# Optimization experiments

Measured on AMD Instinct MI355X. Metric: run time of the kernel, lower is better.

Reference implementation:

```python
import jax, jax.numpy as jnp
import numpy as np

EPS = 1e-6
ROPE_THETA = 10000.0


def rmsnorm(x, w):
    return x * jax.lax.rsqrt(jnp.mean(x * x, axis=-1, keepdims=True) + EPS) * w


def rope(q, k, seq_len, head_dim):
    # rotate-half RoPE. q,k: [b, h, s, d]
    half = head_dim // 2
    inv_freq = 1.0 / (ROPE_THETA ** (jnp.arange(0, half, dtype=jnp.float32) / half))
    t = jnp.arange(seq_len, dtype=jnp.float32)
    freqs = jnp.outer(t, inv_freq)                      # [s, d/2]
    cos = jnp.concatenate([jnp.cos(freqs)] * 2, axis=-1)  # [s, d]
    sin = jnp.concatenate([jnp.sin(freqs)] * 2, axis=-1)

    def rot(x):
        x1, x2 = x[..., :half], x[..., half:]
        return jnp.concatenate([-x2, x1], axis=-1)

    return q * cos + rot(q) * sin, k * cos + rot(k) * sin


def setup_inputs() -> dict:
    key = jax.random.key(0)
    ks = jax.random.split(key, 8)
    B, S, D, E, F = 4, 2048, 1024, 8, 4096
    sd = 0.02
    return {
        "x": jax.random.normal(ks[0], (B, S, D), dtype=jnp.float32),
        "mapped_tokens": jax.random.randint(ks[1], (B, S), 0, E, dtype=jnp.int32),
        "rms1_w": jnp.ones((D,), dtype=jnp.float32),
        "wqkv": jax.random.normal(ks[2], (D, 3 * D), dtype=jnp.float32) * sd,
        "wo": jax.random.normal(ks[3], (D, D), dtype=jnp.float32) * sd,
        "rms2_w": jnp.ones((D,), dtype=jnp.float32),
        "w1": jax.random.normal(ks[4], (E, D, F), dtype=jnp.float32) * sd,
        "w2": jax.random.normal(ks[5], (E, F, D), dtype=jnp.float32) * sd,
    }


def attention(x, wqkv, wo, num_heads=16):
    B, S, D = x.shape
    hd = D // num_heads
    qkv = x @ wqkv                                       # [b, s, 3D]
    q, k, v = jnp.split(qkv, 3, axis=-1)
    def heads(t):
        return t.reshape(B, S, num_heads, hd).transpose(0, 2, 1, 3)  # [b,h,s,d]
    q, k, v = heads(q), heads(k), heads(v)
    q, k = rope(q, k, S, hd)
    scores = jnp.einsum("bhqd,bhkd->bhqk", q, k) / jnp.sqrt(jnp.float32(hd))
    causal = jnp.tril(jnp.ones((S, S), dtype=bool))
    scores = jnp.where(causal, scores, jnp.finfo(scores.dtype).min)
    attn = jax.nn.softmax(scores, axis=-1)
    out = jnp.einsum("bhqk,bhkd->bhqd", attn, v)
    out = out.transpose(0, 2, 1, 3).reshape(B, S, D)
    return out @ wo


def moe_hash_ffn(x, mapped_tokens, w1, w2):
    # hash-routed MoE: each token goes to exactly one expert given by mapped_tokens
    B, S, D = x.shape
    E = w1.shape[0]
    xf = x.reshape(B * S, D)
    mt = mapped_tokens.reshape(B * S)
    out = jnp.zeros_like(xf)
    for e in range(E):  # small fixed expert count
        y = jax.nn.gelu(xf @ w1[e]) @ w2[e]
        out = out + jnp.where((mt == e)[:, None], y, 0.0)
    return out.reshape(B, S, D)


def reference(x, mapped_tokens, rms1_w, wqkv, wo, rms2_w, w1, w2):
    h = x + attention(rmsnorm(x, rms1_w), wqkv, wo)
    out = h + moe_hash_ffn(rmsnorm(h, rms2_w), mapped_tokens, w1, w2)
    return out
```

## Files before the change

### kernel.cpp

```cpp
#include <hip/hip_runtime.h>
#include <hip/hip_bf16.h>
#include <stdint.h>

typedef __hip_bfloat16 bf16;
typedef __attribute__((ext_vector_type(8))) short bf16x8;
typedef __attribute__((ext_vector_type(4))) float f32x4;
typedef __attribute__((ext_vector_type(16))) float f32x16;
typedef unsigned int u32;

static constexpr int Bsz = 4, S = 2048, D = 1024, E = 8, F = 4096, NH = 16, HD = 64;
static constexpr int TOK = Bsz * S;
static constexpr int SLOTS = TOK + E * 256;

#define DEV __device__ __forceinline__

DEV void async16(const bf16* g, bf16* l) {
  __builtin_amdgcn_global_load_lds((const __attribute__((address_space(1))) u32*)g,
                                   (__attribute__((address_space(3))) u32*)l, 16, 0, 0);
}

DEV u32 lds_off(const bf16* p) {
  return (u32)(uintptr_t)(__attribute__((address_space(3))) bf16*)p;
}

DEV bf16x8 dsr128(u32 addr) {
  bf16x8 d;
  asm volatile("ds_read_b128 %0, %1" : "=v"(d) : "v"(addr));
  return d;
}

DEV float gelu_fast(float x) {
  const float z = 0.7978845608028654f * (x + 0.044715f * x * x * x);
  return x / (1.f + __expf(-2.f * z));
}


__global__ void cvt_transpose(const float* __restrict__ in, bf16* __restrict__ out, int R, int C) {
  __shared__ float t[64][65];
  const size_t zoff = (size_t)blockIdx.z * R * C;
  const int c0 = blockIdx.x * 64, r0 = blockIdx.y * 64;
  const int tid = threadIdx.x;
  const int lrow = tid >> 4, lcol = (tid & 15) * 4;
#pragma unroll
  for (int p = 0; p < 4; ++p) {
    const int r = lrow + p * 16;
    const float4 v = *(const float4*)(in + zoff + (size_t)(r0 + r) * C + c0 + lcol);
    t[r][lcol] = v.x; t[r][lcol + 1] = v.y; t[r][lcol + 2] = v.z; t[r][lcol + 3] = v.w;
  }
  __syncthreads();
  const int ow = tid >> 3, je = (tid & 7) * 8;
#pragma unroll
  for (int p = 0; p < 2; ++p) {
    const int oc = ow + p * 32;
    union { bf16x8 v; bf16 b[8]; } o8;
#pragma unroll
    for (int j = 0; j < 8; ++j) o8.b[j] = __float2bfloat16(t[je + j][oc]);
    *(bf16x8*)(out + zoff + (size_t)(c0 + oc) * R + r0 + je) = o8.v;
  }
}

__global__ void rope_tables(float* __restrict__ cosT, float* __restrict__ sinT) {
  const int s = blockIdx.x * 2 + (threadIdx.x >> 5);
  const int i = threadIdx.x & 31;
  const float inv_freq = powf(10000.f, -(float)i / 32.f);
  const float ang = (float)s * inv_freq;
  cosT[s * 32 + i] = cosf(ang);
  sinT[s * 32 + i] = sinf(ang);
}

__global__ void rmsnorm_k(const float* __restrict__ x, const float* __restrict__ w, bf16* __restrict__ out) {
  const size_t row = blockIdx.x;
  const int tid = threadIdx.x;
  const float4 v = *(const float4*)(x + row * D + tid * 4);
  float ss = v.x * v.x + v.y * v.y + v.z * v.z + v.w * v.w;
#pragma unroll
  for (int off = 1; off < 64; off <<= 1) ss += __shfl_xor(ss, off);
  __shared__ float red[4];
  if ((tid & 63) == 0) red[tid >> 6] = ss;
  __syncthreads();
  const float inv = rsqrtf((red[0] + red[1] + red[2] + red[3]) * (1.f / D) + 1e-6f);
  const float4 wv = *(const float4*)(w + tid * 4);
  union { ushort4 u; bf16 b[4]; } o;
  o.b[0] = __float2bfloat16(v.x * inv * wv.x);
  o.b[1] = __float2bfloat16(v.y * inv * wv.y);
  o.b[2] = __float2bfloat16(v.z * inv * wv.z);
  o.b[3] = __float2bfloat16(v.w * inv * wv.w);
  *(ushort4*)((unsigned short*)out + row * D + tid * 4) = o.u;
}

__global__ void route_init(int* counts, int* cursors, int* perm) {
  const int i = blockIdx.x * 256 + threadIdx.x;
  if (i < E) { counts[i] = 0; cursors[i] = 0; }
  if (i < SLOTS) perm[i] = -1;
}
__global__ void route_count(const int* __restrict__ mt, int* counts) {
  const int i = blockIdx.x * 256 + threadIdx.x;
  if (i < TOK) atomicAdd(&counts[mt[i]], 1);
}
__global__ void route_offsets(const int* __restrict__ counts, int* aoff) {
  if (threadIdx.x == 0) {
    int off = 0; aoff[0] = 0;
    for (int e = 0; e < E; ++e) { off += (counts[e] + 255) & ~255; aoff[e + 1] = off; }
  }
}
__global__ void route_scatter(const int* __restrict__ mt, const int* __restrict__ aoff,
                              int* cursors, int* perm) {
  const int i = blockIdx.x * 256 + threadIdx.x;
  if (i < TOK) { const int e = mt[i]; perm[aoff[e] + atomicAdd(&cursors[e], 1)] = i; }
}

__global__ __launch_bounds__(512) void qkv8p(
    const bf16* __restrict__ A, const bf16* __restrict__ Bt,
    const float* __restrict__ c_t, const float* __restrict__ s_t,
    bf16* __restrict__ o_q, bf16* __restrict__ o_k, bf16* __restrict__ o_v) {
  constexpr int K = 1024, NT = K / 64;
  __shared__ __align__(16) bf16 LA[2][256 * 64];
  __shared__ __align__(16) bf16 LB[2][256 * 64];
  const int tid = threadIdx.x;
  const int lane = tid & 63, wv = tid >> 6;
  const int wm = wv >> 2, wn = wv & 3;
  const int rl = lane & 15, kg = lane >> 4;
  const int gx = gridDim.x;
  const int nwg = gx * gridDim.y;
  int bid = blockIdx.y * gx + blockIdx.x;
  bid = (bid & 7) * (nwg >> 3) + (bid >> 3);
  const int nbase = (bid % gx) * 256, mbase = (bid / gx) * 256;
  f32x4 acc[8][4] = {};
  const int srow = tid >> 3;
  const int sc = (tid & 7) ^ ((srow >> 1) & 7);
  const bf16* Ag = A + (size_t)(mbase + srow) * K + sc * 8;
  const bf16* Bg = Bt + (size_t)(nbase + srow) * K + sc * 8;

  auto stage = [&](int t, int h) {
    const int buf = t & 1;
    const int mat = h >> 1, rh = h & 1;
    const bf16* src = (mat ? Bg : Ag) + (size_t)(rh * 128) * K + t * 64;
    bf16* dst = (mat ? &LB[buf][0] : &LA[buf][0]) + rh * 128 * 64 + tid * 8;
    async16(src, dst);
    async16(src + (size_t)64 * K, dst + 64 * 64);
  };

  bf16x8 bfr[4];
  auto phaseC = [&](int t, int ks, int mih, bool loadB) {
    const int buf = t & 1;
    const u32 ab = lds_off(&LA[buf][0]);
    const u32 bb = lds_off(&LB[buf][0]);
    bf16x8 af[4];
#pragma unroll
    for (int mi = 0; mi < 4; ++mi) {
      const int row = wm * 128 + mih * 64 + mi * 16 + rl;
      const u32 ph = (u32)((ks * 4 + kg) ^ ((row >> 1) & 7));
      af[mi] = dsr128(ab + (u32)row * 128 + ph * 16);
    }
    if (loadB) {
#pragma unroll
      for (int ni = 0; ni < 4; ++ni) {
        const int row = wn * 64 + ni * 16 + rl;
        const u32 ph = (u32)((ks * 4 + kg) ^ ((row >> 1) & 7));
        bfr[ni] = dsr128(bb + (u32)row * 128 + ph * 16);
      }
    }
    asm volatile("s_waitcnt lgkmcnt(0)" ::: "memory");
    __builtin_amdgcn_sched_barrier(0);
    __builtin_amdgcn_s_setprio(1);
#pragma unroll
    for (int mi = 0; mi < 4; ++mi)
#pragma unroll
      for (int ni = 0; ni < 4; ++ni)
        acc[mih * 4 + mi][ni] =
            __builtin_amdgcn_mfma_f32_16x16x32_bf16(af[mi], bfr[ni], acc[mih * 4 + mi][ni], 0, 0, 0);
    __builtin_amdgcn_s_setprio(0);
  };

  stage(0, 0); stage(0, 1); stage(0, 2); stage(0, 3);
  for (int t = 0; t < NT; ++t) {
    const bool more = (t + 1 < NT);
#pragma unroll
    for (int p = 0; p < 4; ++p) {
      if (p == 0) {
        if (more) {
          stage(t + 1, 0);
          asm volatile("s_waitcnt vmcnt(2)" ::: "memory");
        } else {
          asm volatile("s_waitcnt vmcnt(0)" ::: "memory");
        }
        __builtin_amdgcn_s_barrier();
        __builtin_amdgcn_sched_barrier(0);
      } else if (more) {
        stage(t + 1, p);
      }
      phaseC(t, p >> 1, p & 1, (p & 1) == 0);
      __builtin_amdgcn_s_barrier();
      __builtin_amdgcn_sched_barrier(0);
    }
  }

  const int colbase = nbase + wn * 64;
  const int part = colbase >> 10;
  const int head = (colbase & 1023) >> 6;
#pragma unroll
  for (int ai = 0; ai < 8; ++ai) {
    const int rowoff = (ai >> 2) * 64 + (ai & 3) * 16;
#pragma unroll
    for (int r = 0; r < 4; ++r) {
      const int grow = mbase + wm * 128 + rowoff + kg * 4 + r;
      const int bb = grow >> 11, sp = grow & (S - 1);
      if (part == 2) {
#pragma unroll
        for (int ni = 0; ni < 4; ++ni) {
          const int d = ni * 16 + rl;
          o_v[((size_t)(bb * NH + head) * HD + d) * S + sp] = __float2bfloat16(acc[ai][ni][r]);
        }
      } else {
        bf16* dst = (part == 0) ? o_q : o_k;
        const size_t base = ((size_t)(bb * NH + head) * S + sp) * HD;
#pragma unroll
        for (int np = 0; np < 2; ++np) {
          const int i = np * 16 + rl;
          const float c = c_t[sp * 32 + i];
          const float sn = s_t[sp * 32 + i];
          const float lo = acc[ai][np][r];
          const float hi = acc[ai][np + 2][r];
          dst[base + i] = __float2bfloat16(lo * c - hi * sn);
          dst[base + i + 32] = __float2bfloat16(hi * c + lo * sn);
        }
      }
    }
  }
}

template <int EPI, int K>
__global__ __launch_bounds__(512) void ffn4p(
    const bf16* __restrict__ A, const bf16* __restrict__ Bt,
    const int* __restrict__ aoff, long long estride,
    bf16* __restrict__ o_act,
    const int* __restrict__ perm, const float* __restrict__ hres,
    float* __restrict__ o_out) {
  constexpr int NT = K / 64;
  __shared__ __align__(16) bf16 LA[2][256 * 64];
  __shared__ __align__(16) bf16 LB[2][256 * 64];
  const int tid = threadIdx.x;
  const int lane = tid & 63, wv = tid >> 6;
  const int wm = wv >> 2, wn = wv & 3;
  const int rl = lane & 15, kg = lane >> 4;
  const int gx = gridDim.x;
  const int nwg = gx * gridDim.y;
  int bid = blockIdx.y * gx + blockIdx.x;
  bid = (bid & 7) * (nwg >> 3) + (bid >> 3);
  const int nbase = (bid % gx) * 256, mbase = (bid / gx) * 256;
  if (mbase >= aoff[E]) return;
  int e = 0;
#pragma unroll
  for (int t = 0; t < E - 1; ++t) e += (mbase >= aoff[t + 1]) ? 1 : 0;
  const bf16* Btp = Bt + (size_t)e * estride;

  f32x4 acc[8][4] = {};
  const int srow = tid >> 3;
  const int sc = (tid & 7) ^ ((srow >> 1) & 7);
  const bf16* Agr[4];
#pragma unroll
  for (int c = 0; c < 4; ++c) {
    int slot = mbase + c * 64 + srow;
    if constexpr (EPI == 2) { const int pt = perm[slot]; slot = (pt < 0) ? 0 : pt; }
    Agr[c] = A + (size_t)slot * K + sc * 8;
  }
  const bf16* Bg = Btp + (size_t)(nbase + srow) * K + sc * 8;

  auto stage = [&](int t, int h) {
    const int buf = t & 1;
    const int mat = h >> 1, rh = h & 1;
    bf16* dst = (mat ? &LB[buf][0] : &LA[buf][0]) + rh * 128 * 64 + tid * 8;
    if (mat == 0) {
      async16(Agr[rh * 2] + t * 64, dst);
      async16(Agr[rh * 2 + 1] + t * 64, dst + 64 * 64);
    } else {
      const bf16* src = Bg + (size_t)(rh * 128) * K + t * 64;
      async16(src, dst);
      async16(src + (size_t)64 * K, dst + 64 * 64);
    }
  };

  bf16x8 bfr[4];
  auto phaseC = [&](int t, int ks, int mih, bool loadB) {
    const int buf = t & 1;
    const u32 ab = lds_off(&LA[buf][0]);
    const u32 bb = lds_off(&LB[buf][0]);
    bf16x8 af[4];
#pragma unroll
    for (int mi = 0; mi < 4; ++mi) {
      const int row = wm * 128 + mih * 64 + mi * 16 + rl;
      const u32 ph = (u32)((ks * 4 + kg) ^ ((row >> 1) & 7));
      af[mi] = dsr128(ab + (u32)row * 128 + ph * 16);
    }
    if (loadB) {
#pragma unroll
      for (int ni = 0; ni < 4; ++ni) {
        const int row = wn * 64 + ni * 16 + rl;
        const u32 ph = (u32)((ks * 4 + kg) ^ ((row >> 1) & 7));
        bfr[ni] = dsr128(bb + (u32)row * 128 + ph * 16);
      }
    }
    asm volatile("s_waitcnt lgkmcnt(0)" ::: "memory");
    __builtin_amdgcn_sched_barrier(0);
    __builtin_amdgcn_s_setprio(1);
#pragma unroll
    for (int mi = 0; mi < 4; ++mi)
#pragma unroll
      for (int ni = 0; ni < 4; ++ni)
        acc[mih * 4 + mi][ni] =
            __builtin_amdgcn_mfma_f32_16x16x32_bf16(af[mi], bfr[ni], acc[mih * 4 + mi][ni], 0, 0, 0);
    __builtin_amdgcn_s_setprio(0);
  };

  stage(0, 0); stage(0, 1); stage(0, 2); stage(0, 3);
  for (int t = 0; t < NT; ++t) {
    const bool more = (t + 1 < NT);
#pragma unroll
    for (int p = 0; p < 4; ++p) {
      if (p == 0) {
        if (more) {
          stage(t + 1, 0);
          asm volatile("s_waitcnt vmcnt(2)" ::: "memory");
        } else {
          asm volatile("s_waitcnt vmcnt(0)" ::: "memory");
        }
        __builtin_amdgcn_s_barrier();
        __builtin_amdgcn_sched_barrier(0);
      } else if (more) {
        stage(t + 1, p);
      }
      phaseC(t, p >> 1, p & 1, (p & 1) == 0);
      __builtin_amdgcn_s_barrier();
      __builtin_amdgcn_sched_barrier(0);
    }
  }

#pragma unroll
  for (int ai = 0; ai < 8; ++ai) {
    const int rowoff = (ai >> 2) * 64 + (ai & 3) * 16;
#pragma unroll
    for (int r = 0; r < 4; ++r) {
      const int grow = mbase + wm * 128 + rowoff + kg * 4 + r;
#pragma unroll
      for (int ni = 0; ni < 4; ++ni) {
        const int gcol = nbase + wn * 64 + ni * 16 + rl;
        const float vv = acc[ai][ni][r];
        if constexpr (EPI == 2) {
          o_act[(size_t)grow * 4096 + gcol] = __float2bfloat16(gelu_fast(vv));
        } else {
          const int tk = perm[grow];
          if (tk >= 0) {
            const size_t ix = (size_t)tk * 1024 + gcol;
            o_out[ix] = hres[ix] + vv;
          }
        }
      }
    }
  }
}

template <int EPI, int BM>
__global__ __launch_bounds__(2 * BM) void gemm_bt(
    const bf16* __restrict__ A, const bf16* __restrict__ Bt, int M, int N, int K,
    const int* __restrict__ aoff, long long estride,
    const float* __restrict__ xres, float* __restrict__ o_h,
    bf16* __restrict__ o_act,
    const int* __restrict__ perm, const float* __restrict__ hres, float* __restrict__ o_out) {
  constexpr int WN = BM / 64;
  constexpr int MR = BM / 2;
  constexpr int M_FR = MR / 16;
  __shared__ __align__(16) bf16 As[2][BM * 32];
  __shared__ __align__(16) bf16 Bs[2][BM * 32];
  const int tid = threadIdx.x;
  const int lane = tid & 63, wv = tid >> 6;
  const int wm = wv / WN, wn = wv % WN;
  const int rl = lane & 15, kg = lane >> 4;
  const int gx = gridDim.x;
  const int nwg = gx * gridDim.y;
  int bid = blockIdx.y * gx + blockIdx.x;
  bid = (bid & 7) * (nwg >> 3) + (bid >> 3);
  const int nbase = (bid % gx) * BM, mbase = (bid / gx) * BM;
  const bf16* Btp = Bt;
  if constexpr (EPI >= 2) {
    int e = 0;
#pragma unroll
    for (int t = 0; t < E - 1; ++t) e += (mbase >= aoff[t + 1]) ? 1 : 0;
    Btp = Bt + (size_t)e * estride;
  }
  f32x4 acc[M_FR][4] = {};
  const int srow = tid >> 2;
  const int sc = (tid & 3) ^ ((srow >> 1) & 3);
  const bf16* Agp[2];
#pragma unroll
  for (int c = 0; c < 2; ++c) {
    int rowslot = mbase + c * MR + srow;
    if constexpr (EPI == 2) {
      const int t = perm[rowslot];
      rowslot = (t < 0) ? 0 : t;
    }
    Agp[c] = A + (size_t)rowslot * K + sc * 8;
  }
  const bf16* Bg = Btp + (size_t)(nbase + srow) * K + sc * 8;

  auto stage = [&](int bi, int ko) {
#pragma unroll
    for (int c = 0; c < 2; ++c) {
      async16(Agp[c] + ko, &As[bi][c * MR * 32 + wv * 512]);
      async16(Bg + (size_t)(c * MR) * K + ko, &Bs[bi][c * MR * 32 + wv * 512]);
    }
  };
  auto compute = [&](int bi) {
    bf16x8 af[M_FR], bfr[4];
#pragma unroll
    for (int mi = 0; mi < M_FR; ++mi) {
      const int row = wm * MR + mi * 16 + rl;
      af[mi] = *(const bf16x8*)&As[bi][row * 32 + ((kg ^ ((row >> 1) & 3))) * 8];
    }
#pragma unroll
    for (int ni = 0; ni < 4; ++ni) {
      const int row = wn * 64 + ni * 16 + rl;
      bfr[ni] = *(const bf16x8*)&Bs[bi][row * 32 + ((kg ^ ((row >> 1) & 3))) * 8];
    }
#pragma unroll
    for (int mi = 0; mi < M_FR; ++mi)
#pragma unroll
      for (int ni = 0; ni < 4; ++ni)
        acc[mi][ni] = __builtin_amdgcn_mfma_f32_16x16x32_bf16(af[mi], bfr[ni], acc[mi][ni], 0, 0, 0);
  };

  const int nk = K >> 5;
  stage(0, 0);
  __syncthreads();
  for (int kb = 0; kb < nk; ++kb) {
    if (kb + 1 < nk) stage((kb + 1) & 1, (kb + 1) * 32);
    compute(kb & 1);
    __syncthreads();
  }

#pragma unroll
  for (int mi = 0; mi < M_FR; ++mi) {
#pragma unroll
    for (int ni = 0; ni < 4; ++ni) {
#pragma unroll
      for (int r = 0; r < 4; ++r) {
        const int grow = mbase + wm * MR + mi * 16 + kg * 4 + r;
        const int gcol = nbase + wn * 64 + ni * 16 + rl;
        const float vv = acc[mi][ni][r];
        if constexpr (EPI == 1) {
          const size_t ix = (size_t)grow * 1024 + gcol;
          o_h[ix] = xres[ix] + vv;
        } else if constexpr (EPI == 2) {
          o_act[(size_t)grow * 4096 + gcol] = __float2bfloat16(gelu_fast(vv));
        } else {
          const int t = perm[grow];
          if (t >= 0) {
            const size_t ix = (size_t)t * 1024 + gcol;
            o_out[ix] = hres[ix] + vv;
          }
        }
      }
    }
  }
}

__global__ __launch_bounds__(128, 4) void attn_kernel(const bf16* __restrict__ Qb,
                                                      const bf16* __restrict__ Kb,
                                                      const bf16* __restrict__ Vt,
                                                      bf16* __restrict__ AO) {
  const int bh = blockIdx.x;
  const int w = threadIdx.x >> 6, lane = threadIdx.x & 63;
  const int q = lane & 31, hi = lane >> 5;
  const bf16* Qp = Qb + (size_t)bh * S * HD;
  const bf16* Kp = Kb + (size_t)bh * S * HD;
  const bf16* Vp = Vt + (size_t)bh * S * HD;
  const int b = bh >> 4, h = bh & 15;
  __shared__ __align__(16) bf16 Pl[2][4][32][16];
  const int qt = (S / 32 - 1) - (blockIdx.y * 2 + w);
  const int qrow0 = qt * 32;
  const float SC = 0.125f * 1.4426950408889634f;
  bf16x8 qf[4];
#pragma unroll
  for (int t = 0; t < 4; ++t)
    qf[t] = *(const bf16x8*)(Qp + (size_t)(qrow0 + q) * HD + t * 16 + hi * 8);
  f32x16 oa0 = {}, oa1 = {};
  float m = -INFINITY, l = 0.f;
  const int nt = (qt + 2) >> 1;
  for (int kt = 0; kt < nt; ++kt) {
    const int kvb = kt * 64;
    f32x16 sa0 = {}, sa1 = {};
#pragma unroll
    for (int t = 0; t < 4; ++t) {
      const bf16x8 kf0 = *(const bf16x8*)(Kp + (size_t)(kvb + q) * HD + t * 16 + hi * 8);
      sa0 = __builtin_amdgcn_mfma_f32_32x32x16_bf16(kf0, qf[t], sa0, 0, 0, 0);
    }
#pragma unroll
    for (int t = 0; t < 4; ++t) {
      const bf16x8 kf1 = *(const bf16x8*)(Kp + (size_t)(kvb + 32 + q) * HD + t * 16 + hi * 8);
      sa1 = __builtin_amdgcn_mfma_f32_32x32x16_bf16(kf1, qf[t], sa1, 0, 0, 0);
    }
#pragma unroll
    for (int r = 0; r < 16; ++r) {
      const int kloc = (r & 3) + 8 * (r >> 2) + 4 * hi;
      sa0[r] = (kvb + kloc > qrow0 + q) ? -3.0e38f : sa0[r] * SC;
      sa1[r] = (kvb + 32 + kloc > qrow0 + q) ? -3.0e38f : sa1[r] * SC;
    }
    float vm;
    {
      float a0 = fmaxf(fmaxf(sa0[0], sa0[1]), fmaxf(sa0[2], sa0[3]));
      float a1 = fmaxf(fmaxf(sa0[4], sa0[5]), fmaxf(sa0[6], sa0[7]));
      float a2 = fmaxf(fmaxf(sa0[8], sa0[9]), fmaxf(sa0[10], sa0[11]));
      float a3 = fmaxf(fmaxf(sa0[12], sa0[13]), fmaxf(sa0[14], sa0[15]));
      float b0 = fmaxf(fmaxf(sa1[0], sa1[1]), fmaxf(sa1[2], sa1[3]));
      float b1 = fmaxf(fmaxf(sa1[4], sa1[5]), fmaxf(sa1[6], sa1[7]));
      float b2 = fmaxf(fmaxf(sa1[8], sa1[9]), fmaxf(sa1[10], sa1[11]));
      float b3 = fmaxf(fmaxf(sa1[12], sa1[13]), fmaxf(sa1[14], sa1[15]));
      vm = fmaxf(fmaxf(fmaxf(a0, a1), fmaxf(a2, a3)), fmaxf(fmaxf(b0, b1), fmaxf(b2, b3)));
    }
    vm = fmaxf(vm, __shfl_xor(vm, 32));
    const bool grow = __any(vm > m);
    const float mn = grow ? fmaxf(m, vm) : m;
#pragma unroll
    for (int r = 0; r < 16; ++r) {
      sa0[r] = exp2f(sa0[r] - mn);
      sa1[r] = exp2f(sa1[r] - mn);
    }
    float ps;
    {
      float a0 = (sa0[0] + sa0[1]) + (sa0[2] + sa0[3]);
      float a1 = (sa0[4] + sa0[5]) + (sa0[6] + sa0[7]);
      float a2 = (sa0[8] + sa0[9]) + (sa0[10] + sa0[11]);
      float a3 = (sa0[12] + sa0[13]) + (sa0[14] + sa0[15]);
      float b0 = (sa1[0] + sa1[1]) + (sa1[2] + sa1[3]);
      float b1 = (sa1[4] + sa1[5]) + (sa1[6] + sa1[7]);
      float b2 = (sa1[8] + sa1[9]) + (sa1[10] + sa1[11]);
      float b3 = (sa1[12] + sa1[13]) + (sa1[14] + sa1[15]);
      ps = ((a0 + a1) + (a2 + a3)) + ((b0 + b1) + (b2 + b3));
    }
    ps += __shfl_xor(ps, 32);
    if (grow) {
      const float scs = exp2f(m - mn);
      l = l * scs + ps;
      m = mn;
#pragma unroll
      for (int r = 0; r < 16; ++r) { oa0[r] *= scs; oa1[r] *= scs; }
    } else {
      l += ps;
    }
#pragma unroll
    for (int g = 0; g < 8; ++g) {
      union { ushort4 u4; bf16 bb[4]; } pk;
#pragma unroll
      for (int j = 0; j < 4; ++j) {
        const int r = 4 * (g & 3) + j;
        pk.bb[j] = __float2bfloat16((g < 4) ? sa0[r] : sa1[r]);
      }
      *(ushort4*)&Pl[w][g >> 1][q][8 * (g & 1) + 4 * hi] = pk.u4;
    }
#pragma unroll
    for (int s2i = 0; s2i < 4; ++s2i) {
      const bf16x8 pf = *(const bf16x8*)&Pl[w][s2i][q][8 * hi];
      const bf16x8 vf0 = *(const bf16x8*)(Vp + (size_t)q * S + kvb + 16 * s2i + 8 * hi);
      const bf16x8 vf1 = *(const bf16x8*)(Vp + (size_t)(32 + q) * S + kvb + 16 * s2i + 8 * hi);
      oa0 = __builtin_amdgcn_mfma_f32_32x32x16_bf16(vf0, pf, oa0, 0, 0, 0);
      oa1 = __builtin_amdgcn_mfma_f32_32x32x16_bf16(vf1, pf, oa1, 0, 0, 0);
    }
  }
  const float invl = 1.f / l;
#pragma unroll
  for (int n = 0; n < 2; ++n) {
#pragma unroll
    for (int g = 0; g < 4; ++g) {
      union { ushort4 u4; bf16 bb[4]; } o4;
#pragma unroll
      for (int mi = 0; mi < 4; ++mi) {
        const float val = (n ? oa1[4 * g + mi] : oa0[4 * g + mi]) * invl;
        o4.bb[mi] = __float2bfloat16(val);
      }
      const int d = n * 32 + 8 * g + 4 * hi;
      *(ushort4*)&AO[((size_t)(b * S + qrow0 + q)) * D + h * HD + d] = o4.u4;
    }
  }
}

extern "C" void kernel_launch(void* const* d_in, const int* in_sizes, int n_in,
                              void* d_out, int out_size, void* d_ws, size_t ws_size,
                              hipStream_t stream) {
  const float* x = (const float*)d_in[0];
  const int* mt = (const int*)d_in[1];
  const float* rms1 = (const float*)d_in[2];
  const float* wqkv = (const float*)d_in[3];
  const float* wo = (const float*)d_in[4];
  const float* rms2 = (const float*)d_in[5];
  const float* w1 = (const float*)d_in[6];
  const float* w2 = (const float*)d_in[7];
  float* out = (float*)d_out;
  (void)in_sizes; (void)n_in; (void)out_size; (void)ws_size;

  char* ws = (char*)d_ws;
  size_t off = 0;
  auto alloc = [&](size_t b) { void* p = ws + off; off = (off + b + 255) & ~(size_t)255; return p; };
  bf16* wqkvT = (bf16*)alloc((size_t)3072 * 1024 * 2);
  bf16* woT   = (bf16*)alloc((size_t)1024 * 1024 * 2);
  bf16* w1T   = (bf16*)alloc((size_t)E * F * D * 2);
  bf16* w2T   = (bf16*)alloc((size_t)E * D * F * 2);
  float* cosT = (float*)alloc((size_t)S * 32 * 4);
  float* sinT = (float*)alloc((size_t)S * 32 * 4);
  float* hbuf = (float*)alloc((size_t)TOK * D * 4);
  bf16* xn2   = (bf16*)alloc((size_t)TOK * D * 2);
  int* counts  = (int*)alloc(E * 4);
  int* cursors = (int*)alloc(E * 4);
  int* aoff    = (int*)alloc((E + 1) * 4);
  int* perm    = (int*)alloc(SLOTS * 4);
  char* R = (char*)alloc((size_t)5 * TOK * D * 2);
  bf16* xn = (bf16*)R;
  bf16* qb = (bf16*)(R + (size_t)1 * TOK * D * 2);
  bf16* kb = (bf16*)(R + (size_t)2 * TOK * D * 2);
  bf16* vb = (bf16*)(R + (size_t)3 * TOK * D * 2);
  bf16* ao = (bf16*)(R + (size_t)4 * TOK * D * 2);
  bf16* act = (bf16*)R;

  cvt_transpose<<<dim3(3072 / 64, 1024 / 64, 1), 256, 0, stream>>>(wqkv, wqkvT, 1024, 3072);
  cvt_transpose<<<dim3(1024 / 64, 1024 / 64, 1), 256, 0, stream>>>(wo, woT, 1024, 1024);
  cvt_transpose<<<dim3(4096 / 64, 1024 / 64, E), 256, 0, stream>>>(w1, w1T, 1024, 4096);
  cvt_transpose<<<dim3(1024 / 64, 4096 / 64, E), 256, 0, stream>>>(w2, w2T, 4096, 1024);
  rope_tables<<<dim3(S / 2), 64, 0, stream>>>(cosT, sinT);
  route_init<<<dim3((SLOTS + 255) / 256), 256, 0, stream>>>(counts, cursors, perm);
  route_count<<<dim3(TOK / 256), 256, 0, stream>>>(mt, counts);
  route_offsets<<<dim3(1), 64, 0, stream>>>(counts, aoff);
  route_scatter<<<dim3(TOK / 256), 256, 0, stream>>>(mt, aoff, cursors, perm);
  rmsnorm_k<<<dim3(TOK), 256, 0, stream>>>(x, rms1, xn);
  qkv8p<<<dim3(3072 / 256, TOK / 256), 512, 0, stream>>>(
      xn, wqkvT, cosT, sinT, qb, kb, vb);
  attn_kernel<<<dim3(64, S / 64), 128, 0, stream>>>(qb, kb, vb, ao);
  gemm_bt<1, 128><<<dim3(1024 / 128, TOK / 128), 256, 0, stream>>>(
      ao, woT, TOK, 1024, 1024, nullptr, 0, x, hbuf, nullptr, nullptr, nullptr, nullptr);
  rmsnorm_k<<<dim3(TOK), 256, 0, stream>>>(hbuf, rms2, xn2);
  ffn4p<2, 1024><<<dim3(4096 / 256, SLOTS / 256), 512, 0, stream>>>(
      xn2, w1T, aoff, (long long)F * D, act, perm, nullptr, nullptr);
  ffn4p<3, 4096><<<dim3(1024 / 256, SLOTS / 256), 512, 0, stream>>>(
      act, w2T, aoff, (long long)D * F, nullptr, perm, hbuf, out);
}
```

Baseline: 708.4 us.

## Split-K FFN down-proj with atomics, reorder GEMM stage pipeline, fold softmax scale into Q

The FFN2 GEMM is split along K into four z-slices. Their partial results are accumulated with float atomicAdd into an output that the Wo GEMM epilogue pre-initialises with the residual, which raises block-level parallelism for the K=4096 GEMM. The qkv and FFN GEMM main loops are restructured to load B first and hold two B fragment register sets, with adjusted vmcnt waits. The attention softmax scale is folded into the Q epilogue, and causal masking is skipped for fully unmasked KV tiles. The atomics add contention and make the summation order nondeterministic.

```diff
diff --git a/kernel.cpp b/kernel.cpp
--- a/kernel.cpp
+++ b/kernel.cpp
@@ -133,15 +133,21 @@
 
   auto stage = [&](int t, int h) {
     const int buf = t & 1;
-    const int mat = h >> 1, rh = h & 1;
-    const bf16* src = (mat ? Bg : Ag) + (size_t)(rh * 128) * K + t * 64;
-    bf16* dst = (mat ? &LB[buf][0] : &LA[buf][0]) + rh * 128 * 64 + tid * 8;
-    async16(src, dst);
-    async16(src + (size_t)64 * K, dst + 64 * 64);
+    if (h < 2) {
+      const bf16* src = Bg + (size_t)(h * 128) * K + t * 64;
+      bf16* dst = &LB[buf][0] + h * 128 * 64 + tid * 8;
+      async16(src, dst);
+      async16(src + (size_t)64 * K, dst + 64 * 64);
+    } else {
+      const int rh = h - 2;
+      const bf16* src = Ag + (size_t)(rh * 64) * K + t * 64;
+      bf16* dst = &LA[buf][0] + rh * 64 * 64 + tid * 8;
+      async16(src, dst);
+      async16(src + (size_t)128 * K, dst + 128 * 64);
+    }
   };
 
-  bf16x8 bfr[4];
-  auto phaseC = [&](int t, int ks, int mih, bool loadB) {
+  auto phaseC = [&](int t, int ks, int mih, bf16x8 (&bfr)[4], bool loadB) {
     const int buf = t & 1;
     const u32 ab = lds_off(&LA[buf][0]);
     const u32 bb = lds_off(&LB[buf][0]);
@@ -172,32 +178,44 @@
     __builtin_amdgcn_s_setprio(0);
   };
 
+  bf16x8 bfr0[4], bfr1[4];
   stage(0, 0); stage(0, 1); stage(0, 2); stage(0, 3);
   for (int t = 0; t < NT; ++t) {
     const bool more = (t + 1 < NT);
-#pragma unroll
-    for (int p = 0; p < 4; ++p) {
-      if (p == 0) {
-        if (more) {
-          stage(t + 1, 0);
-          asm volatile("s_waitcnt vmcnt(2)" ::: "memory");
-        } else {
-          asm volatile("s_waitcnt vmcnt(0)" ::: "memory");
-        }
-        __builtin_amdgcn_s_barrier();
-        __builtin_amdgcn_sched_barrier(0);
-      } else if (more) {
-        stage(t + 1, p);
-      }
-      phaseC(t, p >> 1, p & 1, (p & 1) == 0);
-      __builtin_amdgcn_s_barrier();
-      __builtin_amdgcn_sched_barrier(0);
-    }
+    if (more) {
+      stage(t + 1, 0);
+      asm volatile("s_waitcnt vmcnt(4)" ::: "memory");
+    } else {
+      asm volatile("s_waitcnt vmcnt(2)" ::: "memory");
+    }
+    __builtin_amdgcn_s_barrier();
+    __builtin_amdgcn_sched_barrier(0);
+    phaseC(t, 0, 0, bfr0, true);
+    __builtin_amdgcn_s_barrier();
+    __builtin_amdgcn_sched_barrier(0);
+    if (more) stage(t + 1, 1);
+    phaseC(t, 1, 0, bfr1, true);
+    if (more) {
+      asm volatile("s_waitcnt vmcnt(4)" ::: "memory");
+    } else {
+      asm volatile("s_waitcnt vmcnt(0)" ::: "memory");
+    }
+    __builtin_amdgcn_s_barrier();
+    __builtin_amdgcn_sched_barrier(0);
+    if (more) stage(t + 1, 2);
+    phaseC(t, 0, 1, bfr0, false);
+    __builtin_amdgcn_s_barrier();
+    __builtin_amdgcn_sched_barrier(0);
+    if (more) stage(t + 1, 3);
+    phaseC(t, 1, 1, bfr1, false);
+    __builtin_amdgcn_s_barrier();
+    __builtin_amdgcn_sched_barrier(0);
   }
 
   const int colbase = nbase + wn * 64;
   const int part = colbase >> 10;
   const int head = (colbase & 1023) >> 6;
+  const float qs = (part == 0) ? 0.18033688011112042f : 1.f;
 #pragma unroll
   for (int ai = 0; ai < 8; ++ai) {
     const int rowoff = (ai >> 2) * 64 + (ai & 3) * 16;
@@ -221,8 +239,8 @@
           const float sn = s_t[sp * 32 + i];
           const float lo = acc[ai][np][r];
           const float hi = acc[ai][np + 2][r];
-          dst[base + i] = __float2bfloat16(lo * c - hi * sn);
-          dst[base + i + 32] = __float2bfloat16(hi * c + lo * sn);
+          dst[base + i] = __float2bfloat16((lo * c - hi * sn) * qs);
+          dst[base + i + 32] = __float2bfloat16((hi * c + lo * sn) * qs);
         }
       }
     }
@@ -231,11 +249,10 @@
 
 template <int EPI, int K>
 __global__ __launch_bounds__(512) void ffn4p(
-    const bf16* __restrict__ A, const bf16* __restrict__ Bt,
+    const bf16* __restrict__ A, const bf16* __restrict__ Bt, int lda,
     const int* __restrict__ aoff, long long estride,
     bf16* __restrict__ o_act,
-    const int* __restrict__ perm, const float* __restrict__ hres,
-    float* __restrict__ o_out) {
+    const int* __restrict__ perm, float* __restrict__ o_out) {
   constexpr int NT = K / 64;
   __shared__ __align__(16) bf16 LA[2][256 * 64];
   __shared__ __align__(16) bf16 LB[2][256 * 64];
@@ -249,6 +266,7 @@
   bid = (bid & 7) * (nwg >> 3) + (bid >> 3);
   const int nbase = (bid % gx) * 256, mbase = (bid / gx) * 256;
   if (mbase >= aoff[E]) return;
+  const size_t koff = (size_t)blockIdx.z * K;
   int e = 0;
 #pragma unroll
   for (int t = 0; t < E - 1; ++t) e += (mbase >= aoff[t + 1]) ? 1 : 0;
@@ -262,26 +280,26 @@
   for (int c = 0; c < 4; ++c) {
     int slot = mbase + c * 64 + srow;
     if constexpr (EPI == 2) { const int pt = perm[slot]; slot = (pt < 0) ? 0 : pt; }
-    Agr[c] = A + (size_t)slot * K + sc * 8;
-  }
-  const bf16* Bg = Btp + (size_t)(nbase + srow) * K + sc * 8;
+    Agr[c] = A + (size_t)slot * lda + koff + sc * 8;
+  }
+  const bf16* Bg = Btp + (size_t)(nbase + srow) * lda + koff + sc * 8;
 
   auto stage = [&](int t, int h) {
     const int buf = t & 1;
-    const int mat = h >> 1, rh = h & 1;
-    bf16* dst = (mat ? &LB[buf][0] : &LA[buf][0]) + rh * 128 * 64 + tid * 8;
-    if (mat == 0) {
-      async16(Agr[rh * 2] + t * 64, dst);
-      async16(Agr[rh * 2 + 1] + t * 64, dst + 64 * 64);
+    if (h < 2) {
+      const bf16* src = Bg + (size_t)(h * 128) * lda + t * 64;
+      bf16* dst = &LB[buf][0] + h * 128 * 64 + tid * 8;
+      async16(src, dst);
+      async16(src + (size_t)64 * lda, dst + 64 * 64);
     } else {
-      const bf16* src = Bg + (size_t)(rh * 128) * K + t * 64;
-      async16(src, dst);
-      async16(src + (size_t)64 * K, dst + 64 * 64);
+      const int rh = h - 2;
+      bf16* dst = &LA[buf][0] + rh * 64 * 64 + tid * 8;
+      async16(Agr[rh] + t * 64, dst);
+      async16(Agr[rh + 2] + t * 64, dst + 128 * 64);
     }
   };
 
-  bf16x8 bfr[4];
-  auto phaseC = [&](int t, int ks, int mih, bool loadB) {
+  auto phaseC = [&](int t, int ks, int mih, bf16x8 (&bfr)[4], bool loadB) {
     const int buf = t & 1;
     const u32 ab = lds_off(&LA[buf][0]);
     const u32 bb = lds_off(&LB[buf][0]);
@@ -312,27 +330,38 @@
     __builtin_amdgcn_s_setprio(0);
   };
 
+  bf16x8 bfr0[4], bfr1[4];
   stage(0, 0); stage(0, 1); stage(0, 2); stage(0, 3);
   for (int t = 0; t < NT; ++t) {
     const bool more = (t + 1 < NT);
-#pragma unroll
-    for (int p = 0; p < 4; ++p) {
-      if (p == 0) {
-        if (more) {
-          stage(t + 1, 0);
-          asm volatile("s_waitcnt vmcnt(2)" ::: "memory");
-        } else {
-          asm volatile("s_waitcnt vmcnt(0)" ::: "memory");
-        }
-        __builtin_amdgcn_s_barrier();
-        __builtin_amdgcn_sched_barrier(0);
-      } else if (more) {
-        stage(t + 1, p);
-      }
-      phaseC(t, p >> 1, p & 1, (p & 1) == 0);
-      __builtin_amdgcn_s_barrier();
-      __builtin_amdgcn_sched_barrier(0);
-    }
+    if (more) {
+      stage(t + 1, 0);
+      asm volatile("s_waitcnt vmcnt(4)" ::: "memory");
+    } else {
+      asm volatile("s_waitcnt vmcnt(2)" ::: "memory");
+    }
+    __builtin_amdgcn_s_barrier();
+    __builtin_amdgcn_sched_barrier(0);
+    phaseC(t, 0, 0, bfr0, true);
+    __builtin_amdgcn_s_barrier();
+    __builtin_amdgcn_sched_barrier(0);
+    if (more) stage(t + 1, 1);
+    phaseC(t, 1, 0, bfr1, true);
+    if (more) {
+      asm volatile("s_waitcnt vmcnt(4)" ::: "memory");
+    } else {
+      asm volatile("s_waitcnt vmcnt(0)" ::: "memory");
+    }
+    __builtin_amdgcn_s_barrier();
+    __builtin_amdgcn_sched_barrier(0);
+    if (more) stage(t + 1, 2);
+    phaseC(t, 0, 1, bfr0, false);
+    __builtin_amdgcn_s_barrier();
+    __builtin_amdgcn_sched_barrier(0);
+    if (more) stage(t + 1, 3);
+    phaseC(t, 1, 1, bfr1, false);
+    __builtin_amdgcn_s_barrier();
+    __builtin_amdgcn_sched_barrier(0);
   }
 
 #pragma unroll
@@ -349,10 +378,7 @@
           o_act[(size_t)grow * 4096 + gcol] = __float2bfloat16(gelu_fast(vv));
         } else {
           const int tk = perm[grow];
-          if (tk >= 0) {
-            const size_t ix = (size_t)tk * 1024 + gcol;
-            o_out[ix] = hres[ix] + vv;
-          }
+          if (tk >= 0) atomicAdd(&o_out[(size_t)tk * 1024 + gcol], vv);
         }
       }
     }
@@ -362,10 +388,7 @@
 template <int EPI, int BM>
 __global__ __launch_bounds__(2 * BM) void gemm_bt(
     const bf16* __restrict__ A, const bf16* __restrict__ Bt, int M, int N, int K,
-    const int* __restrict__ aoff, long long estride,
-    const float* __restrict__ xres, float* __restrict__ o_h,
-    bf16* __restrict__ o_act,
-    const int* __restrict__ perm, const float* __restrict__ hres, float* __restrict__ o_out) {
+    const float* __restrict__ xres, float* __restrict__ o_h, float* __restrict__ o_out) {
   constexpr int WN = BM / 64;
   constexpr int MR = BM / 2;
   constexpr int M_FR = MR / 16;
@@ -380,27 +403,13 @@
   int bid = blockIdx.y * gx + blockIdx.x;
   bid = (bid & 7) * (nwg >> 3) + (bid >> 3);
   const int nbase = (bid % gx) * BM, mbase = (bid / gx) * BM;
-  const bf16* Btp = Bt;
-  if constexpr (EPI >= 2) {
-    int e = 0;
-#pragma unroll
-    for (int t = 0; t < E - 1; ++t) e += (mbase >= aoff[t + 1]) ? 1 : 0;
-    Btp = Bt + (size_t)e * estride;
-  }
   f32x4 acc[M_FR][4] = {};
   const int srow = tid >> 2;
   const int sc = (tid & 3) ^ ((srow >> 1) & 3);
   const bf16* Agp[2];
 #pragma unroll
-  for (int c = 0; c < 2; ++c) {
-    int rowslot = mbase + c * MR + srow;
-    if constexpr (EPI == 2) {
-      const int t = perm[rowslot];
-      rowslot = (t < 0) ? 0 : t;
-    }
-    Agp[c] = A + (size_t)rowslot * K + sc * 8;
-  }
-  const bf16* Bg = Btp + (size_t)(nbase + srow) * K + sc * 8;
+  for (int c = 0; c < 2; ++c) Agp[c] = A + (size_t)(mbase + c * MR + srow) * K + sc * 8;
+  const bf16* Bg = Bt + (size_t)(nbase + srow) * K + sc * 8;
 
   auto stage = [&](int bi, int ko) {
 #pragma unroll
@@ -445,19 +454,10 @@
       for (int r = 0; r < 4; ++r) {
         const int grow = mbase + wm * MR + mi * 16 + kg * 4 + r;
         const int gcol = nbase + wn * 64 + ni * 16 + rl;
-        const float vv = acc[mi][ni][r];
-        if constexpr (EPI == 1) {
-          const size_t ix = (size_t)grow * 1024 + gcol;
-          o_h[ix] = xres[ix] + vv;
-        } else if constexpr (EPI == 2) {
-          o_act[(size_t)grow * 4096 + gcol] = __float2bfloat16(gelu_fast(vv));
-        } else {
-          const int t = perm[grow];
-          if (t >= 0) {
-            const size_t ix = (size_t)t * 1024 + gcol;
-            o_out[ix] = hres[ix] + vv;
-          }
-        }
+        const size_t ix = (size_t)grow * 1024 + gcol;
+        const float v = xres[ix] + acc[mi][ni][r];
+        o_h[ix] = v;
+        o_out[ix] = v;
       }
     }
   }
@@ -477,7 +477,6 @@
   __shared__ __align__(16) bf16 Pl[2][4][32][16];
   const int qt = (S / 32 - 1) - (blockIdx.y * 2 + w);
   const int qrow0 = qt * 32;
-  const float SC = 0.125f * 1.4426950408889634f;
   bf16x8 qf[4];
 #pragma unroll
   for (int t = 0; t < 4; ++t)
@@ -498,11 +497,13 @@
       const bf16x8 kf1 = *(const bf16x8*)(Kp + (size_t)(kvb + 32 + q) * HD + t * 16 + hi * 8);
       sa1 = __builtin_amdgcn_mfma_f32_32x32x16_bf16(kf1, qf[t], sa1, 0, 0, 0);
     }
-#pragma unroll
-    for (int r = 0; r < 16; ++r) {
-      const int kloc = (r & 3) + 8 * (r >> 2) + 4 * hi;
-      sa0[r] = (kvb + kloc > qrow0 + q) ? -3.0e38f : sa0[r] * SC;
-      sa1[r] = (kvb + 32 + kloc > qrow0 + q) ? -3.0e38f : sa1[r] * SC;
+    if (kvb + 63 > qrow0) {
+#pragma unroll
+      for (int r = 0; r < 16; ++r) {
+        const int kloc = (r & 3) + 8 * (r >> 2) + 4 * hi;
+        sa0[r] = (kvb + kloc > qrow0 + q) ? -3.0e38f : sa0[r];
+        sa1[r] = (kvb + 32 + kloc > qrow0 + q) ? -3.0e38f : sa1[r];
+      }
     }
     float vm;
     {
@@ -633,10 +634,10 @@
       xn, wqkvT, cosT, sinT, qb, kb, vb);
   attn_kernel<<<dim3(64, S / 64), 128, 0, stream>>>(qb, kb, vb, ao);
   gemm_bt<1, 128><<<dim3(1024 / 128, TOK / 128), 256, 0, stream>>>(
-      ao, woT, TOK, 1024, 1024, nullptr, 0, x, hbuf, nullptr, nullptr, nullptr, nullptr);
+      ao, woT, TOK, 1024, 1024, x, hbuf, out);
   rmsnorm_k<<<dim3(TOK), 256, 0, stream>>>(hbuf, rms2, xn2);
-  ffn4p<2, 1024><<<dim3(4096 / 256, SLOTS / 256), 512, 0, stream>>>(
-      xn2, w1T, aoff, (long long)F * D, act, perm, nullptr, nullptr);
-  ffn4p<3, 4096><<<dim3(1024 / 256, SLOTS / 256), 512, 0, stream>>>(
-      act, w2T, aoff, (long long)D * F, nullptr, perm, hbuf, out);
-}
+  ffn4p<2, 1024><<<dim3(4096 / 256, SLOTS / 256, 1), 512, 0, stream>>>(
+      xn2, w1T, 1024, aoff, (long long)F * D, act, perm, nullptr);
+  ffn4p<3, 1024><<<dim3(1024 / 256, SLOTS / 256, 4), 512, 0, stream>>>(
+      act, w2T, 4096, aoff, (long long)D * F, nullptr, perm, out);
+}
```

Result: slower. 736.9 us (+4.0%).
